# Kernel optimization log

Hardware: AMD Instinct MI355X
Metric: run time of the kernel (lower is better)

Reference implementation:

```python
import jax, jax.numpy as jnp
import numpy as np

T, N, E, CIN, H = 6, 20000, 640000, 3, 64


def setup_inputs() -> dict:
    key = jax.random.key(0)
    ks = jax.random.split(key, 16)
    s = 0.1
    return {
        "node_features": jax.random.normal(ks[0], (T, N, CIN), jnp.float32),
        "edges": jax.random.randint(ks[1], (T, 2, E), 0, N, dtype=jnp.int32),
        # GCN layer 1: in->hidden, GCN layer 2: hidden->hidden
        "W1": s * jax.random.normal(ks[2], (CIN, H), jnp.float32),
        "b1": jnp.zeros((H,), jnp.float32),
        "W2": s * jax.random.normal(ks[3], (H, H), jnp.float32),
        "b2": jnp.zeros((H,), jnp.float32),
        # GRU (torch layout: weight_ih [3H, H_in], weight_hh [3H, H])
        "w_ih": s * jax.random.normal(ks[4], (3 * H, H), jnp.float32),
        "w_hh": s * jax.random.normal(ks[5], (3 * H, H), jnp.float32),
        "b_ih": jnp.zeros((3 * H,), jnp.float32),
        "b_hh": jnp.zeros((3 * H,), jnp.float32),
        # MLP head
        "W3": s * jax.random.normal(ks[6], (H, H), jnp.float32),
        "b3": jnp.zeros((H,), jnp.float32),
        "W4": s * jax.random.normal(ks[7], (H, 1), jnp.float32),
        "b4": jnp.zeros((1,), jnp.float32),
    }


def gcn_conv(x, src, dst, W, b):
    """PyG GCNConv: D^{-1/2}(A+I)D^{-1/2} X W + b, self-loops added."""
    n = x.shape[0]
    deg = jax.ops.segment_sum(jnp.ones(src.shape, x.dtype), dst, num_segments=n) + 1.0
    dinv = jax.lax.rsqrt(deg)  # [N]
    xw = x @ W                 # [N, H]
    norm = dinv[src] * dinv[dst]  # [E]
    agg = jax.ops.segment_sum(xw[src] * norm[:, None], dst, num_segments=n)
    agg = agg + (dinv * dinv)[:, None] * xw  # self-loop term
    return agg + b


def reference(node_features, edges, W1, b1, W2, b2, w_ih, w_hh, b_ih, b_hh, W3, b3, W4, b4):
    n = node_features.shape[1]
    h0 = jnp.zeros((n, H), node_features.dtype)

    def step(h, xs):
        x_t, e_t = xs  # [N,CIN], [2,E]
        src, dst = e_t[0], e_t[1]
        # spatial encode: 2 GCN layers + ReLU (dropout is identity in eval)
        z = jax.nn.relu(gcn_conv(x_t, src, dst, W1, b1))
        z = jax.nn.relu(gcn_conv(z, src, dst, W2, b2))
        # GRU cell (torch semantics)
        gi = z @ w_ih.T + b_ih   # [N, 3H]
        gh = h @ w_hh.T + b_hh   # [N, 3H]
        ir, iz, in_ = jnp.split(gi, 3, axis=-1)
        hr, hz, hn = jnp.split(gh, 3, axis=-1)
        r = jax.nn.sigmoid(ir + hr)
        zg = jax.nn.sigmoid(iz + hz)
        ng = jnp.tanh(in_ + r * hn)
        h_new = (1.0 - zg) * ng + zg * h
        return h_new, None

    h_last, _ = jax.lax.scan(step, h0, (node_features, edges))
    hidden = jax.nn.relu(h_last @ W3 + b3)
    pred = jax.nn.sigmoid(hidden @ W4 + b4)  # [N, 1]
    return pred
```

## Files before the change

kernel.cpp:

```cpp
#include <hip/hip_runtime.h>
#include <math.h>

static constexpr int NN   = 20000;
static constexpr int TT   = 6;
static constexpr int EE   = 640000;
static constexpr int CINC = 3;
static constexpr int HH   = 64;
static constexpr int RBG  = 4;
static constexpr int BKSH = 7;
static constexpr int NBKT = (NN + (1 << BKSH) - 1) >> BKSH;
static constexpr int CAP  = 6144;
static constexpr int EPB  = 4096;
static constexpr int GBLK = 5000;
static constexpr int GTOT = TT * GBLK;
static constexpr int GPX  = GTOT / 8;
static constexpr int G1NPB = 32;
static constexpr int G1BPT = (NN + G1NPB - 1) / G1NPB;
static constexpr int G1TOT = TT * G1BPT;
static constexpr int G1PX  = (G1TOT + 7) / 8;

typedef __attribute__((ext_vector_type(8))) short bf16x8;
typedef __attribute__((ext_vector_type(4))) float f32x4;

__device__ inline unsigned short f2bf(float f) {
    unsigned u = __float_as_uint(f);
    unsigned r = (u + 0x7FFFu + ((u >> 16) & 1u)) >> 16;
    return (unsigned short)r;
}
__device__ inline float bflo(unsigned u) { return __uint_as_float(u << 16); }
__device__ inline float bfhi(unsigned u) { return __uint_as_float(u & 0xFFFF0000u); }

__device__ inline float fsig(float x) {
    return __builtin_amdgcn_rcpf(1.f + __expf(-x));
}
__device__ inline float ftanh(float x) {
    x = fminf(fmaxf(x, -15.f), 15.f);
    float e = __expf(2.f * x);
    return (e - 1.f) * __builtin_amdgcn_rcpf(e + 1.f);
}

__global__ void bin6_kernel(const int* __restrict__ edges, int* __restrict__ gcur,
                            int* __restrict__ bucketArr) {
    int t = blockIdx.y;
    __shared__ int hist[NBKT];
    __shared__ int base[NBKT];
    int tid = threadIdx.x;
    for (int i = tid; i < NBKT; i += 256) hist[i] = 0;
    __syncthreads();
    const int* src = edges + (size_t)t * 2 * EE;
    const int* dst = src + EE;
    int e0 = blockIdx.x * EPB;
    int pack[16], loff[16], bkt[16];
    int m = 0;
#pragma unroll
    for (int i = 0; i < 16; ++i) {
        int e = e0 + tid + i * 256;
        if (e < EE) {
            int s = src[e], d = dst[e];
            int b = d >> BKSH;
            bkt[i] = b;
            pack[i] = ((d & 127) << 16) | s;
            loff[i] = atomicAdd(&hist[b], 1);
            m = i + 1;
        }
    }
    __syncthreads();
    for (int i = tid; i < NBKT; i += 256)
        base[i] = atomicAdd(&gcur[t * NBKT + i], hist[i]);
    __syncthreads();
    for (int i = 0; i < m; ++i) {
        int b = bkt[i];
        int pos = base[b] + loff[i];
        if (pos < CAP)
            bucketArr[(size_t)(t * NBKT + b) * CAP + pos] = pack[i];
    }
}

__global__ void scan_gcur_kernel(const int* __restrict__ gcur, int* __restrict__ gbase,
                                 int* __restrict__ rowptr6) {
    int t = blockIdx.x;
    __shared__ int sv[NBKT];
    int tid = threadIdx.x;
    if (tid < NBKT) sv[tid] = gcur[t * NBKT + tid];
    __syncthreads();
    if (tid == 0) {
        int s = 0;
        for (int i = 0; i < NBKT; ++i) { int v = sv[i]; sv[i] = s; s += v; }
        rowptr6[t * (NN + 1) + NN] = EE;
    }
    __syncthreads();
    if (tid < NBKT) gbase[t * NBKT + tid] = sv[tid];
}

__global__ void regroup6_kernel(const int* __restrict__ gcur, const int* __restrict__ gbase,
                                const int* __restrict__ bucketArr, int* __restrict__ rowptr6,
                                float* __restrict__ dinv6, int* __restrict__ col6) {
    int bk = blockIdx.x, t = blockIdx.y;
    __shared__ int hist[128];
    __shared__ int lscan[128];
    __shared__ int cursor[128];
    __shared__ int lcol[CAP];
    int tid = threadIdx.x;
    if (tid < 128) hist[tid] = 0;
    __syncthreads();
    int ecnt = gcur[t * NBKT + bk];
    if (ecnt > CAP) ecnt = CAP;
    const int* barr = bucketArr + (size_t)(t * NBKT + bk) * CAP;
    for (int e = tid; e < ecnt; e += 256) atomicAdd(&hist[barr[e] >> 16], 1);
    __syncthreads();
    if (tid < 128) lscan[tid] = hist[tid];
    __syncthreads();
    for (int off = 1; off < 128; off <<= 1) {
        int v = 0, a = 0;
        if (tid < 128) { v = lscan[tid]; a = (tid >= off) ? lscan[tid - off] : 0; }
        __syncthreads();
        if (tid < 128) lscan[tid] = v + a;
        __syncthreads();
    }
    int base = gbase[t * NBKT + bk];
    int nb0 = bk << BKSH;
    if (tid < 128) {
        int excl = lscan[tid] - hist[tid];
        cursor[tid] = excl;
        int n = nb0 + tid;
        if (n < NN) {
            rowptr6[t * (NN + 1) + n] = base + excl;
            dinv6[t * NN + n] = rsqrtf((float)hist[tid] + 1.0f);
        }
    }
    __syncthreads();
    for (int e = tid; e < ecnt; e += 256) {
        int w = barr[e];
        int dl = w >> 16, s = w & 0xFFFF;
        int off = atomicAdd(&cursor[dl], 1);
        lcol[off] = s;
    }
    __syncthreads();
    int* colt = col6 + (size_t)t * EE + base;
    for (int e = tid; e < ecnt; e += 256) colt[e] = lcol[e];
}

__global__ void pack_gruh_kernel(const float* __restrict__ whh,
                                 unsigned* __restrict__ Wh01, unsigned short* __restrict__ Whn) {
    int idx = blockIdx.x * blockDim.x + threadIdx.x;
    if (idx >= HH * HH) return;
    int k = idx >> 6, jj = idx & 63;
    unsigned w_hr = f2bf(whh[jj * HH + k]);
    unsigned w_hz = f2bf(whh[(64 + jj) * HH + k]);
    unsigned w_hn = f2bf(whh[(128 + jj) * HH + k]);
    Wh01[idx] = w_hr | (w_hz << 16);
    Whn[idx] = (unsigned short)w_hn;
}

__global__ void pack_bfrag_kernel(const float* __restrict__ wih,
                                  unsigned short* __restrict__ Bfrag) {
    int idx = blockIdx.x * blockDim.x + threadIdx.x;
    if (idx >= 24 * 64 * 8) return;
    int frag = idx >> 9;
    int l    = (idx >> 3) & 63;
    int e    = idx & 7;
    int jt = frag >> 1, kk = frag & 1;
    int j = jt * 16 + (l & 15);
    int k = kk * 32 + ((l >> 4) << 3) + e;
    Bfrag[idx] = f2bf(wih[j * HH + k]);
}

__global__ void pack_bfrag2_kernel(const float* __restrict__ W2,
                                   unsigned short* __restrict__ Bfrag2) {
    int idx = blockIdx.x * blockDim.x + threadIdx.x;
    if (idx >= 8 * 64 * 8) return;
    int frag = idx >> 9;
    int l    = (idx >> 3) & 63;
    int e    = idx & 7;
    int jt = frag >> 1, kk = frag & 1;
    int j = jt * 16 + (l & 15);
    int k = kk * 32 + ((l >> 4) << 3) + e;
    Bfrag2[idx] = f2bf(W2[k * HH + j]);
}

__global__ void xd_kernel(const float* __restrict__ nf, const float* __restrict__ dinv6,
                          float4* __restrict__ xd6) {
    int t = blockIdx.y;
    int n = blockIdx.x * 256 + threadIdx.x;
    if (n >= NN) return;
    const float* xr = nf + (size_t)t * NN * CINC + n * CINC;
    float d = dinv6[t * NN + n];
    xd6[(size_t)t * NN + n] = make_float4(d * xr[0], d * xr[1], d * xr[2], 0.f);
}

__global__ void gather1x_kernel(const int* __restrict__ rowptr6, const int* __restrict__ col6,
                                const float* __restrict__ dinv6, const float4* __restrict__ xd6,
                                float4* __restrict__ agg6) {
    int bid = blockIdx.x;
    int widx = (bid & 7) * G1PX + (bid >> 3);
    if (widx >= G1TOT) return;
    int t = widx / G1BPT;
    int iblk = widx - t * G1BPT;
    const int* rowptr = rowptr6 + t * (NN + 1);
    const int* col = col6 + (size_t)t * EE;
    const float4* xd = xd6 + (size_t)t * NN;
    float4* agg = agg6 + (size_t)t * NN;
    const float* dinv = dinv6 + t * NN;
    int tid = threadIdx.x;
    int node = iblk * G1NPB + (tid >> 3);
    if (node >= NN) return;
    int l = tid & 7;
    int ps = rowptr[node], pe = rowptr[node + 1];
    float ax = 0.f, ay = 0.f, az = 0.f;
    for (int p = ps + l; p < pe; p += 8) {
        float4 v = xd[col[p]];
        ax += v.x; ay += v.y; az += v.z;
    }
    ax += __shfl_xor(ax, 1); ay += __shfl_xor(ay, 1); az += __shfl_xor(az, 1);
    ax += __shfl_xor(ax, 2); ay += __shfl_xor(ay, 2); az += __shfl_xor(az, 2);
    ax += __shfl_xor(ax, 4); ay += __shfl_xor(ay, 4); az += __shfl_xor(az, 4);
    if (l == 0) {
        float4 self = xd[node];
        float d = dinv[node];
        agg[node] = make_float4(d * (ax + self.x), d * (ay + self.y),
                                d * (az + self.z), 0.f);
    }
}

__global__ __launch_bounds__(256) void y2z1_mfma_kernel(
        const float4* __restrict__ agg6, const float* __restrict__ W1,
        const float* __restrict__ b1, const unsigned short* __restrict__ Bfrag2,
        const float* __restrict__ dinv6, unsigned short* __restrict__ Y2all) {
    int w = threadIdx.x >> 6, lane = threadIdx.x & 63;
    int tile = blockIdx.x * 4 + w;
    int m0 = tile << 4;
    int r16 = lane & 15, kg = lane >> 4;
    float4 a = agg6[m0 + r16];
    bf16x8 a0, a1;
#pragma unroll
    for (int e = 0; e < 8; ++e) {
        int k0 = (kg << 3) + e;
        float v0 = b1[k0];
        v0 = fmaf(a.x, W1[0 * HH + k0], v0);
        v0 = fmaf(a.y, W1[1 * HH + k0], v0);
        v0 = fmaf(a.z, W1[2 * HH + k0], v0);
        a0[e] = (short)f2bf(v0 > 0.f ? v0 : 0.f);
        int k1 = 32 + (kg << 3) + e;
        float v1 = b1[k1];
        v1 = fmaf(a.x, W1[0 * HH + k1], v1);
        v1 = fmaf(a.y, W1[1 * HH + k1], v1);
        v1 = fmaf(a.z, W1[2 * HH + k1], v1);
        a1[e] = (short)f2bf(v1 > 0.f ? v1 : 0.f);
    }
    f32x4 acc[4];
#pragma unroll
    for (int jt = 0; jt < 4; ++jt) {
        bf16x8 b0 = *(const bf16x8*)(Bfrag2 + ((size_t)((jt << 1) + 0) << 9) + (lane << 3));
        bf16x8 b1f = *(const bf16x8*)(Bfrag2 + ((size_t)((jt << 1) + 1) << 9) + (lane << 3));
        f32x4 c = {0.f, 0.f, 0.f, 0.f};
        c = __builtin_amdgcn_mfma_f32_16x16x32_bf16(a0, b0, c, 0, 0, 0);
        c = __builtin_amdgcn_mfma_f32_16x16x32_bf16(a1, b1f, c, 0, 0, 0);
        acc[jt] = c;
    }
#pragma unroll
    for (int jt = 0; jt < 4; ++jt) {
#pragma unroll
        for (int reg = 0; reg < 4; ++reg) {
            int m = m0 + (kg << 2) + reg;
            Y2all[((size_t)m << 6) + jt * 16 + r16] = f2bf(acc[jt][reg] * dinv6[m]);
        }
    }
}

__global__ void gather6_kernel(const int* __restrict__ rowptr6, const int* __restrict__ col6,
                               const float* __restrict__ dinv6, const unsigned short* __restrict__ ybase,
                               const float* __restrict__ b, unsigned short* __restrict__ zbase) {
    int bid = blockIdx.x;
    int widx = (bid & 7) * GPX + (bid >> 3);
    int t = widx / GBLK;
    int iblk = widx - t * GBLK;
    const int* rowptr = rowptr6 + t * (NN + 1);
    const int* col = col6 + (size_t)t * EE;
    const float* dinv = dinv6 + t * NN;
    const unsigned char* y = (const unsigned char*)(ybase + (size_t)t * NN * HH);
    unsigned short* z = zbase + (size_t)t * NN * HH;

    int node = (iblk * 256 + threadIdx.x) >> 6;
    if (node >= NN) return;
    int lane = threadIdx.x & 63;
    int g = lane >> 3, q = lane & 7;
    int ps = rowptr[node], pe = rowptr[node + 1];
    unsigned qoff = (unsigned)q << 4;
    float acc[8];
    if (g == 0) {
        const uint4 v = *(const uint4*)(y + (((unsigned)node << 7) + qoff));
        acc[0] = bflo(v.x); acc[1] = bfhi(v.x);
        acc[2] = bflo(v.y); acc[3] = bfhi(v.y);
        acc[4] = bflo(v.z); acc[5] = bfhi(v.z);
        acc[6] = bflo(v.w); acc[7] = bfhi(v.w);
    } else {
#pragma unroll
        for (int j = 0; j < 8; ++j) acc[j] = 0.f;
    }
    for (int p = ps + g; p < pe; p += 8) {
        unsigned c = (unsigned)col[p];
        const uint4 v = *(const uint4*)(y + ((c << 7) + qoff));
        acc[0] += bflo(v.x); acc[1] += bfhi(v.x);
        acc[2] += bflo(v.y); acc[3] += bfhi(v.y);
        acc[4] += bflo(v.z); acc[5] += bfhi(v.z);
        acc[6] += bflo(v.w); acc[7] += bfhi(v.w);
    }
#pragma unroll
    for (int j = 0; j < 8; ++j) {
        acc[j] += __shfl_xor(acc[j], 8);
        acc[j] += __shfl_xor(acc[j], 16);
        acc[j] += __shfl_xor(acc[j], 32);
    }
    if (g == 0) {
        float d = dinv[node];
        const float4 b0 = *(const float4*)(b + (q << 3));
        const float4 b1 = *(const float4*)(b + (q << 3) + 4);
        float o[8];
        o[0] = fmaf(d, acc[0], b0.x); o[1] = fmaf(d, acc[1], b0.y);
        o[2] = fmaf(d, acc[2], b0.z); o[3] = fmaf(d, acc[3], b0.w);
        o[4] = fmaf(d, acc[4], b1.x); o[5] = fmaf(d, acc[5], b1.y);
        o[6] = fmaf(d, acc[6], b1.z); o[7] = fmaf(d, acc[7], b1.w);
#pragma unroll
        for (int j = 0; j < 8; ++j) o[j] = o[j] > 0.f ? o[j] : 0.f;
        uint4 w;
        w.x = (unsigned)f2bf(o[0]) | ((unsigned)f2bf(o[1]) << 16);
        w.y = (unsigned)f2bf(o[2]) | ((unsigned)f2bf(o[3]) << 16);
        w.z = (unsigned)f2bf(o[4]) | ((unsigned)f2bf(o[5]) << 16);
        w.w = (unsigned)f2bf(o[6]) | ((unsigned)f2bf(o[7]) << 16);
        *(uint4*)(z + ((size_t)node << 6) + (q << 3)) = w;
    }
}

__global__ __launch_bounds__(256) void giall_mfma_kernel(
        const unsigned short* __restrict__ Zb6, const unsigned short* __restrict__ Bfrag,
        const float* __restrict__ bih, unsigned short* __restrict__ gi) {
    int w = threadIdx.x >> 6, lane = threadIdx.x & 63;
    int tile = blockIdx.x * 4 + w;
    int m0 = tile << 4;
    int r16 = lane & 15, kg = lane >> 4;
    const unsigned short* zrow = Zb6 + ((size_t)(m0 + r16) << 6) + (kg << 3);
    bf16x8 a0 = *(const bf16x8*)zrow;
    bf16x8 a1 = *(const bf16x8*)(zrow + 32);
    f32x4 acc[12];
#pragma unroll
    for (int jt = 0; jt < 12; ++jt) {
        bf16x8 b0 = *(const bf16x8*)(Bfrag + ((size_t)((jt << 1) + 0) << 9) + (lane << 3));
        bf16x8 b1 = *(const bf16x8*)(Bfrag + ((size_t)((jt << 1) + 1) << 9) + (lane << 3));
        f32x4 c = {0.f, 0.f, 0.f, 0.f};
        c = __builtin_amdgcn_mfma_f32_16x16x32_bf16(a0, b0, c, 0, 0, 0);
        c = __builtin_amdgcn_mfma_f32_16x16x32_bf16(a1, b1, c, 0, 0, 0);
        acc[jt] = c;
    }
#pragma unroll
    for (int jt = 0; jt < 12; ++jt) {
        float bi = bih[jt * 16 + r16];
#pragma unroll
        for (int reg = 0; reg < 4; ++reg) {
            int node = m0 + (kg << 2) + reg;
            gi[(size_t)node * 192 + jt * 16 + r16] = f2bf(acc[jt][reg] + bi);
        }
    }
}

__global__ __launch_bounds__(256) void gru6_kernel(
        const unsigned short* __restrict__ gi,
        const unsigned* __restrict__ Wh01, const unsigned short* __restrict__ Whn,
        const float* __restrict__ bhh,
        const float* __restrict__ W3, const float* __restrict__ b3,
        const float* __restrict__ W4, const float* __restrict__ b4,
        float* __restrict__ out) {
    __shared__ unsigned sW01[HH * HH];
    __shared__ unsigned short sWn[HH * HH];
    __shared__ float hs[4][RBG][HH];
    int tid = threadIdx.x;
    int wid = tid >> 6, lane = tid & 63;
    int nbase = (blockIdx.x * 4 + wid) * RBG;

    for (int i = tid; i < HH * HH; i += 256) { sW01[i] = Wh01[i]; sWn[i] = Whn[i]; }
    __syncthreads();

#pragma unroll
    for (int r = 0; r < RBG; ++r) hs[wid][r][lane] = 0.f;
    float bh0 = bhh[lane], bh1 = bhh[64 + lane], bh2 = bhh[128 + lane];

#pragma unroll 1
    for (int t = 0; t < TT; ++t) {
        float aR[RBG], aZ[RBG], aN[RBG];
#pragma unroll
        for (int r = 0; r < RBG; ++r) { aR[r] = aZ[r] = aN[r] = 0.f; }
#pragma unroll 1
        for (int k0 = 0; k0 < 16; ++k0) {
            float4 hv[RBG];
#pragma unroll
            for (int r = 0; r < RBG; ++r) hv[r] = *(const float4*)(&hs[wid][r][k0 << 2]);
#pragma unroll
            for (int u = 0; u < 4; ++u) {
                int k = k0 * 4 + u;
                unsigned w01 = sW01[(k << 6) + lane];
                float w_hr = bflo(w01), w_hz = bfhi(w01);
                float w_hn = bflo((unsigned)sWn[(k << 6) + lane]);
#pragma unroll
                for (int r = 0; r < RBG; ++r) {
                    float hk = (u == 0) ? hv[r].x : (u == 1) ? hv[r].y
                             : (u == 2) ? hv[r].z : hv[r].w;
                    aR[r] = fmaf(hk, w_hr, aR[r]);
                    aZ[r] = fmaf(hk, w_hz, aZ[r]);
                    aN[r] = fmaf(hk, w_hn, aN[r]);
                }
            }
        }
        const unsigned short* gp = gi + ((size_t)t * NN + nbase) * 192;
#pragma unroll
        for (int r = 0; r < RBG; ++r) {
            size_t gb = (size_t)r * 192;
            float gr = bflo((unsigned)gp[gb + lane]);
            float gz = bflo((unsigned)gp[gb + 64 + lane]);
            float gn = bflo((unsigned)gp[gb + 128 + lane]);
            float rr = fsig(gr + aR[r] + bh0);
            float zz = fsig(gz + aZ[r] + bh1);
            float nn_ = ftanh(gn + rr * (aN[r] + bh2));
            hs[wid][r][lane] = (1.f - zz) * nn_ + zz * hs[wid][r][lane];
        }
    }
    float acc[RBG];
#pragma unroll
    for (int r = 0; r < RBG; ++r) acc[r] = 0.f;
#pragma unroll 1
    for (int k0 = 0; k0 < 16; ++k0) {
        float4 hv[RBG];
#pragma unroll
        for (int r = 0; r < RBG; ++r) hv[r] = *(const float4*)(&hs[wid][r][k0 << 2]);
#pragma unroll
        for (int u = 0; u < 4; ++u) {
            float w = W3[(k0 * 4 + u) * HH + lane];
#pragma unroll
            for (int r = 0; r < RBG; ++r) {
                float hk = (u == 0) ? hv[r].x : (u == 1) ? hv[r].y
                         : (u == 2) ? hv[r].z : hv[r].w;
                acc[r] = fmaf(hk, w, acc[r]);
            }
        }
    }
    float bb = b3[lane], w4 = W4[lane], b40 = b4[0];
#pragma unroll
    for (int r = 0; r < RBG; ++r) {
        float v = acc[r] + bb;
        v = v > 0.f ? v : 0.f;
        float s = v * w4;
        s += __shfl_xor(s, 32); s += __shfl_xor(s, 16); s += __shfl_xor(s, 8);
        s += __shfl_xor(s, 4);  s += __shfl_xor(s, 2);  s += __shfl_xor(s, 1);
        if (lane == r) out[nbase + r] = 1.f / (1.f + expf(-(s + b40)));
    }
}

extern "C" void kernel_launch(void* const* d_in, const int* in_sizes, int n_in,
                              void* d_out, int out_size, void* d_ws, size_t ws_size,
                              hipStream_t stream) {
    const float* nf    = (const float*)d_in[0];
    const int*   edges = (const int*)  d_in[1];
    const float* W1  = (const float*)d_in[2];
    const float* b1  = (const float*)d_in[3];
    const float* W2  = (const float*)d_in[4];
    const float* b2  = (const float*)d_in[5];
    const float* wih = (const float*)d_in[6];
    const float* whh = (const float*)d_in[7];
    const float* bih = (const float*)d_in[8];
    const float* bhh = (const float*)d_in[9];
    const float* W3  = (const float*)d_in[10];
    const float* b3  = (const float*)d_in[11];
    const float* W4  = (const float*)d_in[12];
    const float* b4  = (const float*)d_in[13];
    float* out = (float*)d_out;

    int* wsi      = (int*)d_ws;
    int* gcur     = wsi;
    int* gbase    = gcur + 6 * NBKT;
    int* rowptr6  = gbase + 6 * NBKT;
    int* col6     = rowptr6 + 6 * (NN + 1);
    int* bucketArr= col6 + (size_t)6 * EE;
    uintptr_t fbase = ((uintptr_t)(bucketArr + (size_t)6 * NBKT * CAP) + 15) & ~(uintptr_t)15;
    unsigned short* Bfrag = (unsigned short*)fbase;
    unsigned short* Bfrag2= Bfrag + 24 * 64 * 8;
    unsigned* Wh01= (unsigned*)(Bfrag2 + 8 * 64 * 8);
    unsigned short* Whn = (unsigned short*)(Wh01 + HH * HH);
    float* dinv6 = (float*)(Whn + HH * HH);
    float4* xd6  = (float4*)(dinv6 + 6 * NN + 2);
    float4* agg6 = xd6 + (size_t)6 * NN;
    unsigned short* Y2all = (unsigned short*)(agg6 + (size_t)6 * NN);
    unsigned short* Zb2   = Y2all + (size_t)6 * NN * HH;
    unsigned short* gi    = Zb2 + (size_t)6 * NN * HH;

    const int BS  = 256;
    const int gN  = (NN + BS - 1) / BS;
    const int gG6 = NN / (RBG * 4);
    const int gMM = (TT * NN) / 64;
    const int gBIN = (EE + EPB - 1) / EPB;

    hipMemsetAsync(gcur, 0, 6 * NBKT * sizeof(int), stream);
    pack_gruh_kernel<<<(HH * HH + BS - 1) / BS, BS, 0, stream>>>(whh, Wh01, Whn);
    pack_bfrag_kernel<<<(24 * 64 * 8 + BS - 1) / BS, BS, 0, stream>>>(wih, Bfrag);
    pack_bfrag2_kernel<<<(8 * 64 * 8 + BS - 1) / BS, BS, 0, stream>>>(W2, Bfrag2);

    bin6_kernel<<<dim3(gBIN, TT), BS, 0, stream>>>(edges, gcur, bucketArr);
    scan_gcur_kernel<<<TT, BS, 0, stream>>>(gcur, gbase, rowptr6);
    regroup6_kernel<<<dim3(NBKT, TT), BS, 0, stream>>>(gcur, gbase, bucketArr,
                                                       rowptr6, dinv6, col6);

    xd_kernel<<<dim3(gN, TT), BS, 0, stream>>>(nf, dinv6, xd6);
    gather1x_kernel<<<8 * G1PX, BS, 0, stream>>>(rowptr6, col6, dinv6, xd6, agg6);
    y2z1_mfma_kernel<<<gMM, 256, 0, stream>>>(agg6, W1, b1, Bfrag2, dinv6, Y2all);

    gather6_kernel<<<GTOT, BS, 0, stream>>>(rowptr6, col6, dinv6, Y2all, b2, Zb2);

    giall_mfma_kernel<<<gMM, 256, 0, stream>>>(Zb2, Bfrag, bih, gi);
    gru6_kernel<<<gG6, 256, 0, stream>>>(gi, Wh01, Whn, bhh, W3, b3, W4, b4, out);
}
```

Measured before the change: 240.9 us.

## Use MFMA bf16 matrix cores for GRU recurrent matmul and MLP head

Replaces the scalar-FMA recurrent h@W_hh product in the GRU kernel with 16x16x32 bf16 MFMA instructions. Each 64-thread block now handles 16 nodes, with W_hh pre-packed into MFMA B-fragments in LDS. The W3 MLP head also moves to MFMA, with a shuffle reduction for the W4 dot product. The hidden state is rounded to bf16 before each matmul, which may cost accuracy. The smaller blocks each load the full 24KB weight tile, which adds redundant LDS fill traffic.

```diff
diff --git a/kernel.cpp b/kernel.cpp
--- a/kernel.cpp
+++ b/kernel.cpp
@@ -6,7 +6,6 @@
 static constexpr int EE   = 640000;
 static constexpr int CINC = 3;
 static constexpr int HH   = 64;
-static constexpr int RBG  = 4;
 static constexpr int BKSH = 7;
 static constexpr int NBKT = (NN + (1 << BKSH) - 1) >> BKSH;
 static constexpr int CAP  = 6144;
@@ -140,18 +139,6 @@
     for (int e = tid; e < ecnt; e += 256) colt[e] = lcol[e];
 }
 
-__global__ void pack_gruh_kernel(const float* __restrict__ whh,
-                                 unsigned* __restrict__ Wh01, unsigned short* __restrict__ Whn) {
-    int idx = blockIdx.x * blockDim.x + threadIdx.x;
-    if (idx >= HH * HH) return;
-    int k = idx >> 6, jj = idx & 63;
-    unsigned w_hr = f2bf(whh[jj * HH + k]);
-    unsigned w_hz = f2bf(whh[(64 + jj) * HH + k]);
-    unsigned w_hn = f2bf(whh[(128 + jj) * HH + k]);
-    Wh01[idx] = w_hr | (w_hz << 16);
-    Whn[idx] = (unsigned short)w_hn;
-}
-
 __global__ void pack_bfrag_kernel(const float* __restrict__ wih,
                                   unsigned short* __restrict__ Bfrag) {
     int idx = blockIdx.x * blockDim.x + threadIdx.x;
@@ -176,6 +163,32 @@
     int j = jt * 16 + (l & 15);
     int k = kk * 32 + ((l >> 4) << 3) + e;
     Bfrag2[idx] = f2bf(W2[k * HH + j]);
+}
+
+__global__ void pack_bfragh_kernel(const float* __restrict__ whh,
+                                   unsigned short* __restrict__ Whf) {
+    int idx = blockIdx.x * blockDim.x + threadIdx.x;
+    if (idx >= 24 * 64 * 8) return;
+    int frag = idx >> 9;
+    int l    = (idx >> 3) & 63;
+    int e    = idx & 7;
+    int jt = frag >> 1, kk = frag & 1;
+    int j = jt * 16 + (l & 15);
+    int k = kk * 32 + ((l >> 4) << 3) + e;
+    Whf[idx] = f2bf(whh[j * HH + k]);
+}
+
+__global__ void pack_bfrag3_kernel(const float* __restrict__ W3,
+                                   unsigned short* __restrict__ W3f) {
+    int idx = blockIdx.x * blockDim.x + threadIdx.x;
+    if (idx >= 8 * 64 * 8) return;
+    int frag = idx >> 9;
+    int l    = (idx >> 3) & 63;
+    int e    = idx & 7;
+    int jt = frag >> 1, kk = frag & 1;
+    int j = jt * 16 + (l & 15);
+    int k = kk * 32 + ((l >> 4) << 3) + e;
+    W3f[idx] = f2bf(W3[k * HH + j]);
 }
 
 __global__ void xd_kernel(const float* __restrict__ nf, const float* __restrict__ dinv6,
@@ -362,94 +375,111 @@
     }
 }
 
-__global__ __launch_bounds__(256) void gru6_kernel(
+__global__ __launch_bounds__(64) void gru6_kernel(
         const unsigned short* __restrict__ gi,
-        const unsigned* __restrict__ Wh01, const unsigned short* __restrict__ Whn,
+        const unsigned short* __restrict__ Whf,
         const float* __restrict__ bhh,
-        const float* __restrict__ W3, const float* __restrict__ b3,
+        const unsigned short* __restrict__ W3f, const float* __restrict__ b3,
         const float* __restrict__ W4, const float* __restrict__ b4,
         float* __restrict__ out) {
-    __shared__ unsigned sW01[HH * HH];
-    __shared__ unsigned short sWn[HH * HH];
-    __shared__ float hs[4][RBG][HH];
-    int tid = threadIdx.x;
-    int wid = tid >> 6, lane = tid & 63;
-    int nbase = (blockIdx.x * 4 + wid) * RBG;
-
-    for (int i = tid; i < HH * HH; i += 256) { sW01[i] = Wh01[i]; sWn[i] = Whn[i]; }
-    __syncthreads();
-
-#pragma unroll
-    for (int r = 0; r < RBG; ++r) hs[wid][r][lane] = 0.f;
-    float bh0 = bhh[lane], bh1 = bhh[64 + lane], bh2 = bhh[128 + lane];
+    __shared__ unsigned short sWhf[24 * 64 * 8];
+    __shared__ float hs[16][HH];
+    int l = threadIdx.x;
+    int nbase = blockIdx.x * 16;
+    int r16 = l & 15, kg = l >> 4;
+
+    for (int i = l; i < 1536; i += 64)
+        ((uint4*)sWhf)[i] = ((const uint4*)Whf)[i];
+    for (int i = l; i < 16 * HH; i += 64) ((float*)hs)[i] = 0.f;
+    __syncthreads();
+
+    float bh0[4], bh1[4], bh2[4];
+#pragma unroll
+    for (int jt = 0; jt < 4; ++jt) {
+        bh0[jt] = bhh[jt * 16 + r16];
+        bh1[jt] = bhh[64 + jt * 16 + r16];
+        bh2[jt] = bhh[128 + jt * 16 + r16];
+    }
 
 #pragma unroll 1
     for (int t = 0; t < TT; ++t) {
-        float aR[RBG], aZ[RBG], aN[RBG];
-#pragma unroll
-        for (int r = 0; r < RBG; ++r) { aR[r] = aZ[r] = aN[r] = 0.f; }
-#pragma unroll 1
-        for (int k0 = 0; k0 < 16; ++k0) {
-            float4 hv[RBG];
-#pragma unroll
-            for (int r = 0; r < RBG; ++r) hv[r] = *(const float4*)(&hs[wid][r][k0 << 2]);
-#pragma unroll
-            for (int u = 0; u < 4; ++u) {
-                int k = k0 * 4 + u;
-                unsigned w01 = sW01[(k << 6) + lane];
-                float w_hr = bflo(w01), w_hz = bfhi(w01);
-                float w_hn = bflo((unsigned)sWn[(k << 6) + lane]);
-#pragma unroll
-                for (int r = 0; r < RBG; ++r) {
-                    float hk = (u == 0) ? hv[r].x : (u == 1) ? hv[r].y
-                             : (u == 2) ? hv[r].z : hv[r].w;
-                    aR[r] = fmaf(hk, w_hr, aR[r]);
-                    aZ[r] = fmaf(hk, w_hz, aZ[r]);
-                    aN[r] = fmaf(hk, w_hn, aN[r]);
-                }
+        bf16x8 a0, a1;
+#pragma unroll
+        for (int e = 0; e < 8; ++e) {
+            a0[e] = (short)f2bf(hs[r16][(kg << 3) + e]);
+            a1[e] = (short)f2bf(hs[r16][32 + (kg << 3) + e]);
+        }
+        f32x4 acc[12];
+#pragma unroll
+        for (int jt = 0; jt < 12; ++jt) {
+            bf16x8 b0 = *(const bf16x8*)(sWhf + ((jt << 1) + 0) * 512 + (l << 3));
+            bf16x8 b1 = *(const bf16x8*)(sWhf + ((jt << 1) + 1) * 512 + (l << 3));
+            f32x4 c = {0.f, 0.f, 0.f, 0.f};
+            c = __builtin_amdgcn_mfma_f32_16x16x32_bf16(a0, b0, c, 0, 0, 0);
+            c = __builtin_amdgcn_mfma_f32_16x16x32_bf16(a1, b1, c, 0, 0, 0);
+            acc[jt] = c;
+        }
+        __syncthreads();
+#pragma unroll
+        for (int reg = 0; reg < 4; ++reg) {
+            int nl = (kg << 2) + reg;
+            const unsigned short* gp = gi + ((size_t)t * NN + nbase + nl) * 192;
+#pragma unroll
+            for (int jt = 0; jt < 4; ++jt) {
+                int jj = jt * 16 + r16;
+                float gr = bflo((unsigned)gp[jj]);
+                float gz = bflo((unsigned)gp[64 + jj]);
+                float gn = bflo((unsigned)gp[128 + jj]);
+                float rr = fsig(gr + acc[jt][reg] + bh0[jt]);
+                float zz = fsig(gz + acc[jt + 4][reg] + bh1[jt]);
+                float nn_ = ftanh(gn + rr * (acc[jt + 8][reg] + bh2[jt]));
+                hs[nl][jj] = (1.f - zz) * nn_ + zz * hs[nl][jj];
             }
         }
-        const unsigned short* gp = gi + ((size_t)t * NN + nbase) * 192;
-#pragma unroll
-        for (int r = 0; r < RBG; ++r) {
-            size_t gb = (size_t)r * 192;
-            float gr = bflo((unsigned)gp[gb + lane]);
-            float gz = bflo((unsigned)gp[gb + 64 + lane]);
-            float gn = bflo((unsigned)gp[gb + 128 + lane]);
-            float rr = fsig(gr + aR[r] + bh0);
-            float zz = fsig(gz + aZ[r] + bh1);
-            float nn_ = ftanh(gn + rr * (aN[r] + bh2));
-            hs[wid][r][lane] = (1.f - zz) * nn_ + zz * hs[wid][r][lane];
-        }
-    }
-    float acc[RBG];
-#pragma unroll
-    for (int r = 0; r < RBG; ++r) acc[r] = 0.f;
-#pragma unroll 1
-    for (int k0 = 0; k0 < 16; ++k0) {
-        float4 hv[RBG];
-#pragma unroll
-        for (int r = 0; r < RBG; ++r) hv[r] = *(const float4*)(&hs[wid][r][k0 << 2]);
-#pragma unroll
-        for (int u = 0; u < 4; ++u) {
-            float w = W3[(k0 * 4 + u) * HH + lane];
-#pragma unroll
-            for (int r = 0; r < RBG; ++r) {
-                float hk = (u == 0) ? hv[r].x : (u == 1) ? hv[r].y
-                         : (u == 2) ? hv[r].z : hv[r].w;
-                acc[r] = fmaf(hk, w, acc[r]);
-            }
-        }
-    }
-    float bb = b3[lane], w4 = W4[lane], b40 = b4[0];
-#pragma unroll
-    for (int r = 0; r < RBG; ++r) {
-        float v = acc[r] + bb;
-        v = v > 0.f ? v : 0.f;
-        float s = v * w4;
-        s += __shfl_xor(s, 32); s += __shfl_xor(s, 16); s += __shfl_xor(s, 8);
-        s += __shfl_xor(s, 4);  s += __shfl_xor(s, 2);  s += __shfl_xor(s, 1);
-        if (lane == r) out[nbase + r] = 1.f / (1.f + expf(-(s + b40)));
+        __syncthreads();
+    }
+
+    bf16x8 a0, a1;
+#pragma unroll
+    for (int e = 0; e < 8; ++e) {
+        a0[e] = (short)f2bf(hs[r16][(kg << 3) + e]);
+        a1[e] = (short)f2bf(hs[r16][32 + (kg << 3) + e]);
+    }
+    f32x4 accH[4];
+#pragma unroll
+    for (int jt = 0; jt < 4; ++jt) {
+        bf16x8 b0 = *(const bf16x8*)(W3f + ((size_t)((jt << 1) + 0) << 9) + (l << 3));
+        bf16x8 b1 = *(const bf16x8*)(W3f + ((size_t)((jt << 1) + 1) << 9) + (l << 3));
+        f32x4 c = {0.f, 0.f, 0.f, 0.f};
+        c = __builtin_amdgcn_mfma_f32_16x16x32_bf16(a0, b0, c, 0, 0, 0);
+        c = __builtin_amdgcn_mfma_f32_16x16x32_bf16(a1, b1, c, 0, 0, 0);
+        accH[jt] = c;
+    }
+    float p[4];
+#pragma unroll
+    for (int reg = 0; reg < 4; ++reg) {
+        float s = 0.f;
+#pragma unroll
+        for (int jt = 0; jt < 4; ++jt) {
+            int j = jt * 16 + r16;
+            float v = accH[jt][reg] + b3[j];
+            v = v > 0.f ? v : 0.f;
+            s = fmaf(v, W4[j], s);
+        }
+        p[reg] = s;
+    }
+#pragma unroll
+    for (int reg = 0; reg < 4; ++reg) {
+        p[reg] += __shfl_xor(p[reg], 1);
+        p[reg] += __shfl_xor(p[reg], 2);
+        p[reg] += __shfl_xor(p[reg], 4);
+        p[reg] += __shfl_xor(p[reg], 8);
+    }
+    if (r16 == 0) {
+        float b40 = b4[0];
+#pragma unroll
+        for (int reg = 0; reg < 4; ++reg)
+            out[nbase + (kg << 2) + reg] = 1.f / (1.f + expf(-(p[reg] + b40)));
     }
 }
 
@@ -481,9 +511,9 @@
     uintptr_t fbase = ((uintptr_t)(bucketArr + (size_t)6 * NBKT * CAP) + 15) & ~(uintptr_t)15;
     unsigned short* Bfrag = (unsigned short*)fbase;
     unsigned short* Bfrag2= Bfrag + 24 * 64 * 8;
-    unsigned* Wh01= (unsigned*)(Bfrag2 + 8 * 64 * 8);
-    unsigned short* Whn = (unsigned short*)(Wh01 + HH * HH);
-    float* dinv6 = (float*)(Whn + HH * HH);
+    unsigned short* Whf   = Bfrag2 + 8 * 64 * 8;
+    unsigned short* W3f   = Whf + 24 * 64 * 8;
+    float* dinv6 = (float*)(W3f + 8 * 64 * 8);
     float4* xd6  = (float4*)(dinv6 + 6 * NN + 2);
     float4* agg6 = xd6 + (size_t)6 * NN;
     unsigned short* Y2all = (unsigned short*)(agg6 + (size_t)6 * NN);
@@ -492,14 +522,15 @@
 
     const int BS  = 256;
     const int gN  = (NN + BS - 1) / BS;
-    const int gG6 = NN / (RBG * 4);
+    const int gG6 = NN / 16;
     const int gMM = (TT * NN) / 64;
     const int gBIN = (EE + EPB - 1) / EPB;
 
     hipMemsetAsync(gcur, 0, 6 * NBKT * sizeof(int), stream);
-    pack_gruh_kernel<<<(HH * HH + BS - 1) / BS, BS, 0, stream>>>(whh, Wh01, Whn);
     pack_bfrag_kernel<<<(24 * 64 * 8 + BS - 1) / BS, BS, 0, stream>>>(wih, Bfrag);
     pack_bfrag2_kernel<<<(8 * 64 * 8 + BS - 1) / BS, BS, 0, stream>>>(W2, Bfrag2);
+    pack_bfragh_kernel<<<(24 * 64 * 8 + BS - 1) / BS, BS, 0, stream>>>(whh, Whf);
+    pack_bfrag3_kernel<<<(8 * 64 * 8 + BS - 1) / BS, BS, 0, stream>>>(W3, W3f);
 
     bin6_kernel<<<dim3(gBIN, TT), BS, 0, stream>>>(edges, gcur, bucketArr);
     scan_gcur_kernel<<<TT, BS, 0, stream>>>(gcur, gbase, rowptr6);
@@ -513,5 +544,5 @@
     gather6_kernel<<<GTOT, BS, 0, stream>>>(rowptr6, col6, dinv6, Y2all, b2, Zb2);
 
     giall_mfma_kernel<<<gMM, 256, 0, stream>>>(Zb2, Bfrag, bih, gi);
-    gru6_kernel<<<gG6, 256, 0, stream>>>(gi, Wh01, Whn, bhh, W3, b3, W4, b4, out);
-}
+    gru6_kernel<<<gG6, 64, 0, stream>>>(gi, Whf, bhh, W3f, b3, W4, b4, out);
+}
```

Measured after the change: 207.3 us. 13.9% less time.
